# Optimization experiments

Hardware: AMD Instinct MI355X
Metric: run time of the kernel (lower is better)

The kernel has to match this reference:

```python
import jax, jax.numpy as jnp
import numpy as np

# --- fake-quant helpers with straight-through estimator (STE) ---

def _ste(x, xq):
    # identity grad through the rounding
    return x + jax.lax.stop_gradient(xq - x)

def act_quant(x, bit=2):
    # symmetric per-tensor uniform fake-quant of activations
    n = float(2 ** (bit - 1) - 1)  # 2-bit -> 1 level each side
    s = jnp.max(jnp.abs(x)) + 1e-8
    xq = jnp.round(jnp.clip(x / s, -1.0, 1.0) * n) / n * s
    return _ste(x, xq)

def weight_quant(w, bit=2):
    # DoReFa-style low-bit weight fake-quant
    levels = float(2 ** bit - 1)
    wt = jnp.tanh(w)
    wt = wt / (jnp.max(jnp.abs(wt)) + 1e-8)        # in [-1, 1]
    wq = 2.0 * (jnp.round((wt + 1.0) * 0.5 * levels) / levels) - 1.0
    return _ste(wt, wq)

def conv3x3(x, w, b):
    # NCHW, OIHW, stride 1, padding 1
    y = jax.lax.conv_general_dilated(
        x, w, window_strides=(1, 1), padding=((1, 1), (1, 1)),
        dimension_numbers=("NCHW", "OIHW", "NCHW"))
    return y + b[None, :, None, None]


def setup_inputs() -> dict:
    key = jax.random.key(0)
    k1, k2, k3, k4, k5 = jax.random.split(key, 5)
    B, C, H, W = 16, 64, 128, 128
    fan_in = C * 3 * 3
    std = 1.0 / np.sqrt(fan_in)
    return {
        "x": jax.random.normal(k1, (B, C, H, W), dtype=jnp.float32),
        "w1": jax.random.normal(k2, (C, C, 3, 3), dtype=jnp.float32) * std,
        "b1": jax.random.normal(k3, (C,), dtype=jnp.float32) * std,
        "w2": jax.random.normal(k4, (C, C, 3, 3), dtype=jnp.float32) * std,
        "b2": jax.random.normal(k5, (C,), dtype=jnp.float32) * std,
    }


def reference(x, w1, b1, w2, b2):
    A_BIT, W_BIT, RES_SCALE = 2, 2, 1.0
    out = act_quant(x, A_BIT)                 # quant1
    out = conv3x3(out, weight_quant(w1, W_BIT), b1)  # conv1 (low-bit)
    out1 = jax.nn.relu(out)                   # act
    out1 = act_quant(out1, A_BIT)             # quant2
    res = conv3x3(out1, weight_quant(w2, W_BIT), b2) # conv2 (low-bit)
    return res * RES_SCALE + x                # scaled residual add
```

## Files before the change

kernel.cpp:

```cpp
#include <hip/hip_runtime.h>
#include <math.h>

#define NB 16
#define CC 64
#define HH 128
#define WW 128
#define NPIX (NB*CC*HH*WW)
#define WELEM (CC*CC*9)

#define TRR 8
#define TCC 16
#define HRR 10
#define HCC 18
#define HPX (HRR*HCC)
#define PL  (HH*WW)

#define PYY 132
#define PXX 130
#define XQIMG (PYY*PXX*64)

#define S2OFF 512

typedef __attribute__((ext_vector_type(4))) int   int32x4;
typedef __attribute__((ext_vector_type(8))) short short8_t;

__device__ __forceinline__ int lds_a(int pix, int q) {
    return pix * 64 + ((q ^ ((pix >> 1) & 3)) << 4);
}

__device__ __forceinline__ float read_s1(const unsigned* scal) {
    float m = 0.f;
    #pragma unroll
    for (int i = 0; i < 32; ++i) m = fmaxf(m, __uint_as_float(scal[i * 16]));
    return m + 1e-8f;
}

__device__ __forceinline__ float max4(float4 v) {
    return fmaxf(fmaxf(fabsf(v.x), fabsf(v.y)), fmaxf(fabsf(v.z), fabsf(v.w)));
}

__global__ __launch_bounds__(256) void k_reduce(const float* __restrict__ x,
                                                const float* __restrict__ w1,
                                                const float* __restrict__ w2,
                                                unsigned* __restrict__ scal,
                                                signed char* __restrict__ o1,
                                                signed char* __restrict__ o2,
                                                signed char* __restrict__ xq) {
    __shared__ float red[4];
    const int tid = threadIdx.x;
    if (blockIdx.x < 2048) {
        const float4* x4 = (const float4*)x;
        const int base = blockIdx.x * 2048 + tid;
        float4 v0 = x4[base];
        float4 v1 = x4[base + 256];
        float4 v2 = x4[base + 512];
        float4 v3 = x4[base + 768];
        float4 v4 = x4[base + 1024];
        float4 v5 = x4[base + 1280];
        float4 v6 = x4[base + 1536];
        float4 v7 = x4[base + 1792];
        float a0 = fmaxf(max4(v0), max4(v1));
        float a1 = fmaxf(max4(v2), max4(v3));
        float a2 = fmaxf(max4(v4), max4(v5));
        float a3 = fmaxf(max4(v6), max4(v7));
        float m = fmaxf(fmaxf(a0, a1), fmaxf(a2, a3));
        #pragma unroll
        for (int o = 32; o; o >>= 1) m = fmaxf(m, __shfl_down(m, o, 64));
        if ((tid & 63) == 0) red[tid >> 6] = m;
        __syncthreads();
        if (tid == 0) {
            float v = fmaxf(fmaxf(red[0], red[1]), fmaxf(red[2], red[3]));
            atomicMax(&scal[(blockIdx.x & 31) * 16], __float_as_uint(v));
        }
    } else if (blockIdx.x < 2080) {
        const int wb = blockIdx.x - 2048;
        const int ten = wb >> 4;
        const int sl  = wb & 15;
        const float* __restrict__ w = ten ? w2 : w1;
        signed char* __restrict__ w8 = ten ? o2 : o1;

        const float4* w4 = (const float4*)w;
        float m = 0.f;
        #pragma unroll
        for (int k = 0; k < 9; ++k) {
            float4 a = w4[tid + (k * 4 + 0) * 256];
            float4 b = w4[tid + (k * 4 + 1) * 256];
            float4 c = w4[tid + (k * 4 + 2) * 256];
            float4 d = w4[tid + (k * 4 + 3) * 256];
            m = fmaxf(m, fmaxf(fmaxf(max4(a), max4(b)), fmaxf(max4(c), max4(d))));
        }
        #pragma unroll
        for (int o = 32; o; o >>= 1) m = fmaxf(m, __shfl_down(m, o, 64));
        if ((tid & 63) == 0) red[tid >> 6] = m;
        __syncthreads();
        float mx = fmaxf(fmaxf(red[0], red[1]), fmaxf(red[2], red[3]));
        float inv = 1.f / (tanhf(mx) + 1e-8f);

        #pragma unroll
        for (int j = 0; j < 9; ++j) {
            int i = sl * 2304 + j * 256 + tid;
            float wt = tanhf(w[i]) * inv;
            float r  = rintf((wt + 1.f) * 1.5f);
            int oc = i / 576, rem = i % 576, ic = rem / 9, tap = rem % 9;
            int lane2 = (oc & 15) | ((ic >> 4) << 4);
            w8[(((oc >> 4) * 9 + tap) * 64 + lane2) * 16 + (ic & 15)] =
                (signed char)(int)(2.f * r - 3.f);
        }
    } else {
        const int n = blockIdx.x - 2080;
        for (int t = tid; t < 776; t += 256) {
            int r, c;
            if (t < 520) {
                int r4 = t / 130;
                r = (r4 == 0) ? 0 : 128 + r4;
                c = t - r4 * 130;
            } else {
                int u = t - 520;
                r = 1 + (u >> 1);
                c = (u & 1) ? 129 : 0;
            }
            int4* dst = (int4*)(xq + ((size_t)n * PYY + r) * (PXX * 64)
                                   + (size_t)c * 64);
            int4 z = {0, 0, 0, 0};
            dst[0] = z; dst[1] = z; dst[2] = z; dst[3] = z;
        }
    }
}

__global__ __launch_bounds__(256) void k_quantx(const float* __restrict__ x,
                                                const unsigned* __restrict__ scal,
                                                signed char* __restrict__ xq) {
    __shared__ signed char ldsA[64 * 68];
    __shared__ int ldsB[64 * 16];
    const int tid = threadIdx.x;
    const int n = blockIdx.z, y = blockIdx.y, s = blockIdx.x;
    const float inv_s1 = 1.f / read_s1(scal);

    {
        const int ic = tid >> 2, g = tid & 3;
        const float* __restrict__ src =
            x + (((size_t)n * CC + ic) * HH + y) * WW + s * 64 + g * 16;
        unsigned dw[4];
        #pragma unroll
        for (int q = 0; q < 4; ++q) {
            float4 v = *(const float4*)(src + q * 4);
            float e[4] = {v.x, v.y, v.z, v.w};
            unsigned d = 0;
            #pragma unroll
            for (int j = 0; j < 4; ++j) {
                int qq = (int)rintf(fminf(fmaxf(e[j] * inv_s1, -1.f), 1.f));
                d |= (unsigned)(qq & 255) << (8 * j);
            }
            dw[q] = d;
        }
        *(int4*)(ldsA + ic * 68 + g * 16) = *(const int4*)dw;
    }
    __syncthreads();
    #pragma unroll
    for (int i = 0; i < 4; ++i) {
        int idx = tid + i * 256;
        int d = idx & 15, p = idx >> 4;
        const signed char* a = ldsA + (d * 4) * 68 + p;
        unsigned b0 = (unsigned char)a[0];
        unsigned b1 = (unsigned char)a[68];
        unsigned b2 = (unsigned char)a[136];
        unsigned b3 = (unsigned char)a[204];
        ldsB[p * 16 + d] = (int)(b0 | (b1 << 8) | (b2 << 16) | (b3 << 24));
    }
    __syncthreads();
    signed char* dst = xq + ((size_t)n * PYY + (y + 1)) * (PXX * 64)
                          + (size_t)(1 + s * 64) * 64;
    ((int4*)dst)[tid] = ((const int4*)ldsB)[tid];
}

__global__ __launch_bounds__(256, 5) void k_conv1(
    const signed char* __restrict__ xq,
    const signed char* __restrict__ w8,
    const float* __restrict__ bias,
    unsigned* __restrict__ scal,
    short* __restrict__ accout)
{
    __shared__ float redm[4];
    const int tid = threadIdx.x;
    const int bid = blockIdx.x;
    const int swz = (bid & 7) * 256 + (bid >> 3);
    const int tx  = swz & 7;
    const int ty  = (swz >> 3) & 15;
    const int n   = swz >> 7;
    const int oy0 = ty * TRR;
    const int ox0 = tx * TCC;
    const float s1 = read_s1(scal);

    const int w     = tid >> 6;
    const int lane  = tid & 63;
    const int lq    = lane >> 4;
    const int lc    = lane & 15;
    const int rbase = w * 2;

    const signed char* __restrict__ A0 = xq + (size_t)n * XQIMG
        + ((size_t)(oy0 + rbase) * PXX + ox0 + lc) * 64 + lq * 16;
    const signed char* __restrict__ W0 = w8 + (size_t)lane * 16;

    int32x4 acc[2][4] = {};
    #pragma unroll
    for (int tap = 0; tap < 9; ++tap) {
        const int ky = tap / 3, kx = tap % 3;
        int32x4 b0 = *(const int32x4*)(W0 + (size_t)(0 * 9 + tap) * 1024);
        int32x4 b1 = *(const int32x4*)(W0 + (size_t)(1 * 9 + tap) * 1024);
        int32x4 b2 = *(const int32x4*)(W0 + (size_t)(2 * 9 + tap) * 1024);
        int32x4 b3 = *(const int32x4*)(W0 + (size_t)(3 * 9 + tap) * 1024);
        const signed char* ar = A0 + (ky * PXX + kx) * 64;
        #pragma unroll
        for (int j = 0; j < 2; ++j) {
            int32x4 a = *(const int32x4*)(ar + j * (PXX * 64));
            acc[j][0] = __builtin_amdgcn_mfma_i32_16x16x64_i8(a, b0, acc[j][0], 0, 0, 0);
            acc[j][1] = __builtin_amdgcn_mfma_i32_16x16x64_i8(a, b1, acc[j][1], 0, 0, 0);
            acc[j][2] = __builtin_amdgcn_mfma_i32_16x16x64_i8(a, b2, acc[j][2], 0, 0, 0);
            acc[j][3] = __builtin_amdgcn_mfma_i32_16x16x64_i8(a, b3, acc[j][3], 0, 0, 0);
        }
    }

    const float sc = s1 * (1.f / 3.f);
    float m2 = 0.f;
    #pragma unroll
    for (int j = 0; j < 2; ++j) {
        const int yy = oy0 + rbase + j;
        const size_t pbase = (((size_t)n * HH + yy) * WW + (ox0 + lq * 4)) * 64;
        #pragma unroll
        for (int g = 0; g < 4; ++g) {
            const float bo = bias[g * 16 + lc];
            #pragma unroll
            for (int e = 0; e < 4; ++e) {
                int v = acc[j][g][e];
                m2 = fmaxf(m2, sc * (float)v + bo);
                accout[pbase + (size_t)e * 64 + g * 16 + lc] = (short)v;
            }
        }
    }
    #pragma unroll
    for (int o = 32; o; o >>= 1) m2 = fmaxf(m2, __shfl_down(m2, o, 64));
    if (lane == 0) redm[w] = m2;
    __syncthreads();
    if (tid == 0) {
        float v = fmaxf(fmaxf(redm[0], redm[1]), fmaxf(redm[2], redm[3]));
        atomicMax(&scal[S2OFF + (swz & 7) * 32], __float_as_uint(v));
    }
}

__device__ __forceinline__ bool stage_load(const short* __restrict__ accin,
    int n, int oy0, int ox0, int sr, int scx, bool sact, short8_t ld[8]) {
    int y  = oy0 - 1 + sr;
    int xx = ox0 - 1 + scx;
    bool v = sact & (y >= 0) & (y < HH) & (xx >= 0) & (xx < WW);
    int yc = v ? y : 0, xc = v ? xx : 0;
    const short8_t* __restrict__ ap =
        (const short8_t*)(accin + (((size_t)n * HH + yc) * WW + xc) * 64);
    #pragma unroll
    for (int k = 0; k < 8; ++k) ld[k] = ap[k];
    return v;
}

__device__ __forceinline__ void binarize_store(signed char* sbuf, int tid,
    const short8_t ld[8], bool v, const float* __restrict__ b1v,
    float sc1, float half_s2) {
    unsigned pk[16];
    #pragma unroll
    for (int d = 0; d < 16; ++d) pk[d] = 0;
    if (v) {
        #pragma unroll
        for (int k = 0; k < 8; ++k) {
            short8_t sv = ld[k];
            float4 bA = *(const float4*)(b1v + k * 8);
            float4 bB = *(const float4*)(b1v + k * 8 + 4);
            float ba[8] = {bA.x, bA.y, bA.z, bA.w, bB.x, bB.y, bB.z, bB.w};
            #pragma unroll
            for (int e = 0; e < 8; ++e) {
                float fv = sc1 * (float)sv[e] + ba[e];
                if (fv >= half_s2) pk[2 * k + (e >> 2)] |= 1u << ((e & 3) * 8);
            }
        }
    }
    #pragma unroll
    for (int q = 0; q < 4; ++q) {
        int4 wv;
        wv.x = (int)pk[4 * q];     wv.y = (int)pk[4 * q + 1];
        wv.z = (int)pk[4 * q + 2]; wv.w = (int)pk[4 * q + 3];
        *(int4*)(sbuf + lds_a(tid, q)) = wv;
    }
}

__device__ __forceinline__ void conv2_mfma(const signed char* __restrict__ sbuf,
    const signed char* __restrict__ W0, int rbase, int lq, int lc,
    int32x4 acc[2][4]) {
    #pragma unroll 3
    for (int tap = 0; tap < 9; ++tap) {
        const int ky = tap / 3, kx = tap % 3;
        int32x4 b0 = *(const int32x4*)(W0 + (size_t)(0 * 9 + tap) * 1024);
        int32x4 b1 = *(const int32x4*)(W0 + (size_t)(1 * 9 + tap) * 1024);
        int32x4 b2 = *(const int32x4*)(W0 + (size_t)(2 * 9 + tap) * 1024);
        int32x4 b3 = *(const int32x4*)(W0 + (size_t)(3 * 9 + tap) * 1024);
        #pragma unroll
        for (int j = 0; j < 2; ++j) {
            int pix = (rbase + j + ky) * HCC + kx + lc;
            int32x4 a = *(const int32x4*)(sbuf + lds_a(pix, lq));
            acc[j][0] = __builtin_amdgcn_mfma_i32_16x16x64_i8(a, b0, acc[j][0], 0, 0, 0);
            acc[j][1] = __builtin_amdgcn_mfma_i32_16x16x64_i8(a, b1, acc[j][1], 0, 0, 0);
            acc[j][2] = __builtin_amdgcn_mfma_i32_16x16x64_i8(a, b2, acc[j][2], 0, 0, 0);
            acc[j][3] = __builtin_amdgcn_mfma_i32_16x16x64_i8(a, b3, acc[j][3], 0, 0, 0);
        }
    }
}

__device__ __forceinline__ void conv2_epi_load(const float* __restrict__ x,
    int n, int oy0, int ox0, int rbase, int lq, int lc, float4 xpre[8]) {
    const size_t imgbase = (size_t)n * CC * PL;
    #pragma unroll
    for (int j = 0; j < 2; ++j) {
        const int yy = oy0 + rbase + j;
        const int xb = ox0 + lq * 4;
        #pragma unroll
        for (int g = 0; g < 4; ++g) {
            const int oc = g * 16 + lc;
            xpre[j * 4 + g] =
                *(const float4*)(x + imgbase + (size_t)oc * PL + yy * WW + xb);
        }
    }
}

__device__ __forceinline__ void conv2_epi_store(float* __restrict__ out,
    const float* __restrict__ bias, float sc,
    int n, int oy0, int ox0, int rbase, int lq, int lc,
    const int32x4 acc[2][4], const float4 xpre[8]) {
    const size_t imgbase = (size_t)n * CC * PL;
    #pragma unroll
    for (int j = 0; j < 2; ++j) {
        const int yy = oy0 + rbase + j;
        const int xb = ox0 + lq * 4;
        #pragma unroll
        for (int g = 0; g < 4; ++g) {
            const int oc = g * 16 + lc;
            const float bo = bias[oc];
            const float4 xa = xpre[j * 4 + g];
            size_t p = imgbase + (size_t)oc * PL + yy * WW + xb;
            float4 r;
            r.x = sc * (float)acc[j][g][0] + bo + xa.x;
            r.y = sc * (float)acc[j][g][1] + bo + xa.y;
            r.z = sc * (float)acc[j][g][2] + bo + xa.z;
            r.w = sc * (float)acc[j][g][3] + bo + xa.w;
            *(float4*)(out + p) = r;
        }
    }
}

__global__ __launch_bounds__(256, 4) void k_conv2(
    const float* __restrict__ x,
    const short* __restrict__ accin,
    const signed char* __restrict__ w8,
    const float* __restrict__ bias,
    const float* __restrict__ b1v,
    const unsigned* __restrict__ scal,
    float* __restrict__ out)
{
    __shared__ signed char sA0[HPX * 64] __attribute__((aligned(16)));
    __shared__ signed char sA1[HPX * 64] __attribute__((aligned(16)));

    const int tid = threadIdx.x;
    const int bid = blockIdx.x;
    const int swz = (bid & 7) * 128 + (bid >> 3);
    const int tx  = swz & 7;
    const int typ = (swz >> 3) & 7;
    const int n   = swz >> 6;
    const int ox0 = tx * TCC;
    const int oyA = typ * 16;
    const int oyB = oyA + 8;

    const float s1 = read_s1(scal);
    float mx = 0.f;
    #pragma unroll
    for (int i = 0; i < 8; ++i) mx = fmaxf(mx, __uint_as_float(scal[S2OFF + i * 32]));
    const float s2v = mx + 1e-8f;
    const float half_s2 = 0.5f * s2v;
    const float sc1 = s1 * (1.f / 3.f);
    const float sc  = s2v * (1.f / 3.f);

    const int w     = tid >> 6;
    const int lane  = tid & 63;
    const int lq    = lane >> 4;
    const int lc    = lane & 15;
    const int rbase = w * 2;
    const int sr  = tid / HCC;
    const int scx = tid - sr * HCC;
    const bool sact = tid < HPX;
    const signed char* __restrict__ W0 = w8 + (size_t)lane * 16;

    short8_t ld[8];
    float4 xpre[8];
    bool v0 = stage_load(accin, n, oyA, ox0, sr, scx, sact, ld);
    if (sact) binarize_store(sA0, tid, ld, v0, b1v, sc1, half_s2);
    __syncthreads();

    bool v1 = stage_load(accin, n, oyB, ox0, sr, scx, sact, ld);
    conv2_epi_load(x, n, oyA, ox0, rbase, lq, lc, xpre);
    {
        int32x4 acc[2][4] = {};
        conv2_mfma(sA0, W0, rbase, lq, lc, acc);
        if (sact) binarize_store(sA1, tid, ld, v1, b1v, sc1, half_s2);
        conv2_epi_store(out, bias, sc, n, oyA, ox0, rbase, lq, lc, acc, xpre);
    }
    __syncthreads();
    conv2_epi_load(x, n, oyB, ox0, rbase, lq, lc, xpre);
    {
        int32x4 acc[2][4] = {};
        conv2_mfma(sA1, W0, rbase, lq, lc, acc);
        conv2_epi_store(out, bias, sc, n, oyB, ox0, rbase, lq, lc, acc, xpre);
    }
}

extern "C" void kernel_launch(void* const* d_in, const int* in_sizes, int n_in,
                              void* d_out, int out_size, void* d_ws, size_t ws_size,
                              hipStream_t stream) {
    const float* x  = (const float*)d_in[0];
    const float* w1 = (const float*)d_in[1];
    const float* b1 = (const float*)d_in[2];
    const float* w2 = (const float*)d_in[3];
    const float* b2 = (const float*)d_in[4];
    float* out = (float*)d_out;

    unsigned*    scal  = (unsigned*)d_ws;
    signed char* w8_1  = (signed char*)d_ws + 4096;
    signed char* w8_2  = w8_1 + WELEM;
    short*       acc16 = (short*)((char*)d_ws + 131072);
    signed char* xq    = (signed char*)d_out;

    hipMemsetAsync(d_ws, 0, 4096, stream);

    k_reduce<<<2096, 256, 0, stream>>>(x, w1, w2, scal, w8_1, w8_2, xq);
    k_quantx<<<dim3(2, HH, NB), 256, 0, stream>>>(x, scal, xq);
    k_conv1<<<2048, 256, 0, stream>>>(xq, w8_1, b1, scal, acc16);
    k_conv2<<<1024, 256, 0, stream>>>(x, acc16, w8_2, b2, b1, scal, out);
}
```

Measured before the change: 112.3 us.

## Reorder reduce blocks, swap MFMA operands for vector stores, unpipeline conv2 staging

Weight-quant and pad-zeroing blocks in the reduce kernel now get the lowest block indices so they are scheduled first. Conv1's MFMA operands are swapped so each lane holds four consecutive output channels, which lets the int16 accumulator store become one 8-byte vector write per group and the bias a float4 load. The conv1 tap loop is only partially unrolled to cut register pressure. The conv2 kernel no longer overlaps the second tile's staging loads with the first tile's MFMA, scoping buffers to reduce live registers at the cost of lost overlap.

```diff
diff --git a/kernel.cpp b/kernel.cpp
--- a/kernel.cpp
+++ b/kernel.cpp
@@ -22,6 +22,7 @@
 #define S2OFF 512
 
 typedef __attribute__((ext_vector_type(4))) int   int32x4;
+typedef __attribute__((ext_vector_type(4))) short short4_t;
 typedef __attribute__((ext_vector_type(8))) short short8_t;
 
 __device__ __forceinline__ int lds_a(int pix, int q) {
@@ -48,9 +49,9 @@
                                                 signed char* __restrict__ xq) {
     __shared__ float red[4];
     const int tid = threadIdx.x;
-    if (blockIdx.x < 2048) {
+    if (blockIdx.x >= 48) {
         const float4* x4 = (const float4*)x;
-        const int base = blockIdx.x * 2048 + tid;
+        const int base = (blockIdx.x - 48) * 2048 + tid;
         float4 v0 = x4[base];
         float4 v1 = x4[base + 256];
         float4 v2 = x4[base + 512];
@@ -72,8 +73,8 @@
             float v = fmaxf(fmaxf(red[0], red[1]), fmaxf(red[2], red[3]));
             atomicMax(&scal[(blockIdx.x & 31) * 16], __float_as_uint(v));
         }
-    } else if (blockIdx.x < 2080) {
-        const int wb = blockIdx.x - 2048;
+    } else if (blockIdx.x < 32) {
+        const int wb = blockIdx.x;
         const int ten = wb >> 4;
         const int sl  = wb & 15;
         const float* __restrict__ w = ten ? w2 : w1;
@@ -107,7 +108,7 @@
                 (signed char)(int)(2.f * r - 3.f);
         }
     } else {
-        const int n = blockIdx.x - 2080;
+        const int n = blockIdx.x - 32;
         for (int t = tid; t < 776; t += 256) {
             int r, c;
             if (t < 520) {
@@ -202,7 +203,7 @@
     const signed char* __restrict__ W0 = w8 + (size_t)lane * 16;
 
     int32x4 acc[2][4] = {};
-    #pragma unroll
+    #pragma unroll 3
     for (int tap = 0; tap < 9; ++tap) {
         const int ky = tap / 3, kx = tap % 3;
         int32x4 b0 = *(const int32x4*)(W0 + (size_t)(0 * 9 + tap) * 1024);
@@ -213,10 +214,10 @@
         #pragma unroll
         for (int j = 0; j < 2; ++j) {
             int32x4 a = *(const int32x4*)(ar + j * (PXX * 64));
-            acc[j][0] = __builtin_amdgcn_mfma_i32_16x16x64_i8(a, b0, acc[j][0], 0, 0, 0);
-            acc[j][1] = __builtin_amdgcn_mfma_i32_16x16x64_i8(a, b1, acc[j][1], 0, 0, 0);
-            acc[j][2] = __builtin_amdgcn_mfma_i32_16x16x64_i8(a, b2, acc[j][2], 0, 0, 0);
-            acc[j][3] = __builtin_amdgcn_mfma_i32_16x16x64_i8(a, b3, acc[j][3], 0, 0, 0);
+            acc[j][0] = __builtin_amdgcn_mfma_i32_16x16x64_i8(b0, a, acc[j][0], 0, 0, 0);
+            acc[j][1] = __builtin_amdgcn_mfma_i32_16x16x64_i8(b1, a, acc[j][1], 0, 0, 0);
+            acc[j][2] = __builtin_amdgcn_mfma_i32_16x16x64_i8(b2, a, acc[j][2], 0, 0, 0);
+            acc[j][3] = __builtin_amdgcn_mfma_i32_16x16x64_i8(b3, a, acc[j][3], 0, 0, 0);
         }
     }
 
@@ -225,16 +226,19 @@
     #pragma unroll
     for (int j = 0; j < 2; ++j) {
         const int yy = oy0 + rbase + j;
-        const size_t pbase = (((size_t)n * HH + yy) * WW + (ox0 + lq * 4)) * 64;
+        const size_t pbase = (((size_t)n * HH + yy) * WW + (ox0 + lc)) * 64;
         #pragma unroll
         for (int g = 0; g < 4; ++g) {
-            const float bo = bias[g * 16 + lc];
+            float4 b4 = *(const float4*)(bias + g * 16 + lq * 4);
+            float bv[4] = {b4.x, b4.y, b4.z, b4.w};
+            short4_t s4;
             #pragma unroll
             for (int e = 0; e < 4; ++e) {
                 int v = acc[j][g][e];
-                m2 = fmaxf(m2, sc * (float)v + bo);
-                accout[pbase + (size_t)e * 64 + g * 16 + lc] = (short)v;
+                m2 = fmaxf(m2, sc * (float)v + bv[e]);
+                s4[e] = (short)v;
             }
+            *(short4_t*)(accout + pbase + g * 16 + lq * 4) = s4;
         }
     }
     #pragma unroll
@@ -393,23 +397,30 @@
     const bool sact = tid < HPX;
     const signed char* __restrict__ W0 = w8 + (size_t)lane * 16;
 
-    short8_t ld[8];
-    float4 xpre[8];
-    bool v0 = stage_load(accin, n, oyA, ox0, sr, scx, sact, ld);
-    if (sact) binarize_store(sA0, tid, ld, v0, b1v, sc1, half_s2);
+    {
+        short8_t ld[8];
+        bool v0 = stage_load(accin, n, oyA, ox0, sr, scx, sact, ld);
+        if (sact) binarize_store(sA0, tid, ld, v0, b1v, sc1, half_s2);
+    }
     __syncthreads();
 
-    bool v1 = stage_load(accin, n, oyB, ox0, sr, scx, sact, ld);
-    conv2_epi_load(x, n, oyA, ox0, rbase, lq, lc, xpre);
     {
+        float4 xpre[8];
+        conv2_epi_load(x, n, oyA, ox0, rbase, lq, lc, xpre);
         int32x4 acc[2][4] = {};
         conv2_mfma(sA0, W0, rbase, lq, lc, acc);
+        conv2_epi_store(out, bias, sc, n, oyA, ox0, rbase, lq, lc, acc, xpre);
+    }
+    {
+        short8_t ld[8];
+        bool v1 = stage_load(accin, n, oyB, ox0, sr, scx, sact, ld);
         if (sact) binarize_store(sA1, tid, ld, v1, b1v, sc1, half_s2);
-        conv2_epi_store(out, bias, sc, n, oyA, ox0, rbase, lq, lc, acc, xpre);
     }
     __syncthreads();
-    conv2_epi_load(x, n, oyB, ox0, rbase, lq, lc, xpre);
+
     {
+        float4 xpre[8];
+        conv2_epi_load(x, n, oyB, ox0, rbase, lq, lc, xpre);
         int32x4 acc[2][4] = {};
         conv2_mfma(sA1, W0, rbase, lq, lc, acc);
         conv2_epi_store(out, bias, sc, n, oyB, ox0, rbase, lq, lc, acc, xpre);
```

After: 108.9 us. -3.0%, faster.
